# Kernel tuning notes

Hardware: AMD Instinct MI355X
Metric: run time of the kernel (lower is better)

## Reference

```python
import jax, jax.numpy as jnp
import numpy as np

B, D, H, E = 8192, 1024, 4096, 4
LN_EPS = 1e-5


def setup_inputs() -> dict:
    key = jax.random.key(0)
    ks = jax.random.split(key, 10)
    s_gate = 1.0 / np.sqrt(D)
    s1 = 1.0 / np.sqrt(D)
    s2 = 1.0 / np.sqrt(H)
    return {
        "x": jax.random.normal(ks[0], (B, D), dtype=jnp.float32),
        "gate_w": jax.random.uniform(ks[1], (E, D), jnp.float32, -s_gate, s_gate),
        "gate_b": jax.random.uniform(ks[2], (E,), jnp.float32, -s_gate, s_gate),
        "ln_w": jnp.ones((E, D), jnp.float32),
        "ln_b": jnp.zeros((E, D), jnp.float32),
        "w1": jax.random.uniform(ks[3], (E, D, H), jnp.float32, -s1, s1),
        "b1": jax.random.uniform(ks[4], (E, H), jnp.float32, -s1, s1),
        "w2": jax.random.uniform(ks[5], (E, H, D), jnp.float32, -s2, s2),
        "b2": jax.random.uniform(ks[6], (E, D), jnp.float32, -s2, s2),
        "top_k": 2,
    }


def reference(x, gate_w, gate_b, ln_w, ln_b, w1, b1, w2, b2, top_k):
    n_experts = gate_w.shape[0]
    # gating (eval mode: no noise)
    logits = x @ gate_w.T + gate_b            # (B, E)
    probs = jax.nn.softmax(logits, axis=-1)   # (B, E)
    top_w, top_idx = jax.lax.top_k(probs, top_k)  # (B, k)
    top_w = top_w / (jnp.sum(top_w, axis=-1, keepdims=True) + 1e-9)

    # per-expert LayerNorm: shared normalization, per-expert affine
    mu = jnp.mean(x, axis=-1, keepdims=True)
    var = jnp.var(x, axis=-1, keepdims=True)
    xn = (x - mu) * jax.lax.rsqrt(var + LN_EPS)          # (B, D)
    xe = xn[:, None, :] * ln_w[None] + ln_b[None]        # (B, E, D)

    # dense expert MLPs (GELU exact, matching torch nn.GELU default)
    h = jnp.einsum('bed,edh->beh', xe, w1) + b1[None]    # (B, E, H)
    h = jax.nn.gelu(h, approximate=False)
    stacked = jnp.einsum('beh,ehd->bed', h, w2) + b2[None]  # (B, E, D)

    # gather top-k experts and combine
    gathered = jnp.take_along_axis(stacked, top_idx[:, :, None], axis=1)  # (B, k, D)
    y = jnp.sum(gathered * top_w[:, :, None], axis=1)   # (B, D)

    # Switch load-balancing aux loss
    one_hot = jax.nn.one_hot(top_idx, n_experts, dtype=jnp.float32)  # (B, k, E)
    dispatch_frac = jnp.sum(one_hot, axis=(0, 1)) / (x.shape[0] * top_k)
    mean_prob = jnp.mean(probs, axis=0)
    aux = n_experts * jnp.sum(dispatch_frac * mean_prob)

    return y, probs, top_idx, top_w, aux
```

## Files before the change

kernel.cpp:

```cpp
#include <hip/hip_runtime.h>
#include <hip/hip_bf16.h>
#include <math.h>

#define BB 8192
#define DD 1024
#define HH 4096
#define EE 4
#define NT 132
#define CAP (NT * 128)

typedef __attribute__((ext_vector_type(8))) __bf16 bf16x8;
typedef __attribute__((ext_vector_type(4))) float f32x4;

__device__ __forceinline__ unsigned short f2bf(float f) {
    union { float f; unsigned u; } c; c.f = f;
    unsigned u = c.u;
    unsigned r = (u + 0x7FFFu + ((u >> 16) & 1u)) >> 16;
    return (unsigned short)r;
}

__device__ __forceinline__ void load_lds16(const void* g, void* l) {
    __builtin_amdgcn_global_load_lds(
        (const __attribute__((address_space(1))) void*)g,
        (__attribute__((address_space(3))) void*)l, 16, 0, 0);
}

template <int R, int C>
__global__ void k_prep(const float* __restrict__ src, unsigned short* __restrict__ dst) {
    __shared__ unsigned short tileT[64 * 72];
    const int e = blockIdx.z;
    const int r0 = blockIdx.y * 64, c0 = blockIdx.x * 64;
    const float* s = src + (size_t)e * R * C;
    unsigned short* d = dst + (size_t)e * R * C;
    const int tid = threadIdx.x;
    const int cc = (tid & 15) * 4;
#pragma unroll
    for (int it = 0; it < 4; ++it) {
        int rr = (tid >> 4) + it * 16;
        float4 v = *(const float4*)(s + (size_t)(r0 + rr) * C + c0 + cc);
        tileT[(cc + 0) * 72 + rr] = f2bf(v.x);
        tileT[(cc + 1) * 72 + rr] = f2bf(v.y);
        tileT[(cc + 2) * 72 + rr] = f2bf(v.z);
        tileT[(cc + 3) * 72 + rr] = f2bf(v.w);
    }
    __syncthreads();
#pragma unroll
    for (int it = 0; it < 2; ++it) {
        int chunk = tid + it * 256;
        int cl = chunk >> 3, rl = (chunk & 7) * 8;
        uint4 vv = *(const uint4*)&tileT[cl * 72 + rl];
        *(uint4*)(d + (size_t)(c0 + cl) * R + r0 + rl) = vv;
    }
}

__global__ __launch_bounds__(256) void k_gate(
        const float* __restrict__ x, const float* __restrict__ gw,
        const float* __restrict__ gb,
        float* __restrict__ mu, float* __restrict__ rstd,
        int* __restrict__ cnt, int* __restrict__ rows_tmp,
        float* __restrict__ wts_tmp,
        float* __restrict__ probs_out, float* __restrict__ idx_out,
        float* __restrict__ w_out) {
    const int tid = threadIdx.x;
    const int lane = tid & 63, wv = tid >> 6;
    __shared__ int   s_e[64];
    __shared__ float s_w[64];
    __shared__ int   s_pos[64];
    __shared__ int   s_base[4];

    for (int i = 0; i < 8; ++i) {
        const int rloc = wv * 8 + i;
        const int r = blockIdx.x * 32 + rloc;
        float l0 = 0, l1 = 0, l2 = 0, l3 = 0, s = 0, ss = 0;
#pragma unroll
        for (int k = 0; k < 4; ++k) {
            const int off = k * 256 + lane * 4;
            float4 xv = *(const float4*)(x + (size_t)r * DD + off);
            s  += xv.x + xv.y + xv.z + xv.w;
            ss += xv.x * xv.x + xv.y * xv.y + xv.z * xv.z + xv.w * xv.w;
            float4 g0 = *(const float4*)(gw + 0 * DD + off);
            float4 g1 = *(const float4*)(gw + 1 * DD + off);
            float4 g2 = *(const float4*)(gw + 2 * DD + off);
            float4 g3 = *(const float4*)(gw + 3 * DD + off);
            l0 += xv.x * g0.x + xv.y * g0.y + xv.z * g0.z + xv.w * g0.w;
            l1 += xv.x * g1.x + xv.y * g1.y + xv.z * g1.z + xv.w * g1.w;
            l2 += xv.x * g2.x + xv.y * g2.y + xv.z * g2.z + xv.w * g2.w;
            l3 += xv.x * g3.x + xv.y * g3.y + xv.z * g3.z + xv.w * g3.w;
        }
#pragma unroll
        for (int off = 32; off > 0; off >>= 1) {
            l0 += __shfl_xor(l0, off, 64);
            l1 += __shfl_xor(l1, off, 64);
            l2 += __shfl_xor(l2, off, 64);
            l3 += __shfl_xor(l3, off, 64);
            s  += __shfl_xor(s,  off, 64);
            ss += __shfl_xor(ss, off, 64);
        }
        if (lane == 0) {
            float m = s * (1.0f / DD);
            float var = ss * (1.0f / DD) - m * m;
            mu[r] = m;
            rstd[r] = rsqrtf(var + 1e-5f);
            float lg[4] = { l0 + gb[0], l1 + gb[1], l2 + gb[2], l3 + gb[3] };
            float mx = fmaxf(fmaxf(lg[0], lg[1]), fmaxf(lg[2], lg[3]));
            float p[4], tot = 0.f;
#pragma unroll
            for (int e = 0; e < 4; ++e) { p[e] = __expf(lg[e] - mx); tot += p[e]; }
            float inv = 1.0f / tot;
#pragma unroll
            for (int e = 0; e < 4; ++e) { p[e] *= inv; probs_out[(size_t)r * 4 + e] = p[e]; }
            int e0 = 0; float p0 = p[0];
#pragma unroll
            for (int e = 1; e < 4; ++e) if (p[e] > p0) { p0 = p[e]; e0 = e; }
            int e1 = -1; float p1 = -1.f;
#pragma unroll
            for (int e = 0; e < 4; ++e) if (e != e0 && p[e] > p1) { p1 = p[e]; e1 = e; }
            float s2 = 1.0f / (p0 + p1 + 1e-9f);
            float w0 = p0 * s2, w1v = p1 * s2;
            idx_out[r * 2 + 0] = (float)e0;
            idx_out[r * 2 + 1] = (float)e1;
            w_out[r * 2 + 0] = w0;
            w_out[r * 2 + 1] = w1v;
            s_e[rloc * 2 + 0] = e0; s_w[rloc * 2 + 0] = w0;
            s_e[rloc * 2 + 1] = e1; s_w[rloc * 2 + 1] = w1v;
        }
    }
    __syncthreads();
    if (tid < 4) {
        int c = 0;
        for (int k = 0; k < 64; ++k)
            if (s_e[k] == tid) s_pos[k] = c++;
        s_base[tid] = atomicAdd(cnt + tid, c);
    }
    __syncthreads();
    if (tid < 64) {
        int e = s_e[tid];
        int p = s_base[e] + s_pos[tid];
        int r = blockIdx.x * 32 + (tid >> 1);
        rows_tmp[e * BB + p] = r;
        wts_tmp[e * BB + p] = s_w[tid];
    }
}

__global__ void k_aux(const float* __restrict__ probs, const int* __restrict__ cnt,
                      int* __restrict__ aoff, int* __restrict__ tile_e,
                      float* __restrict__ aux_out) {
    const int tid = threadIdx.x;
    float s0 = 0, s1 = 0, s2 = 0, s3 = 0;
    for (int r = tid; r < BB; r += 256) {
        float4 p = *(const float4*)(probs + (size_t)r * 4);
        s0 += p.x; s1 += p.y; s2 += p.z; s3 += p.w;
    }
    __shared__ float red[4][256];
    red[0][tid] = s0; red[1][tid] = s1; red[2][tid] = s2; red[3][tid] = s3;
    __syncthreads();
    for (int off = 128; off > 0; off >>= 1) {
        if (tid < off) {
#pragma unroll
            for (int q = 0; q < 4; ++q) red[q][tid] += red[q][tid + off];
        }
        __syncthreads();
    }
    if (tid == 0) {
        float aux = 0.f;
        for (int e = 0; e < 4; ++e) {
            float mean_p = red[e][0] * (1.0f / BB);
            float frac = (float)cnt[e] * (1.0f / (BB * 2));
            aux += frac * mean_p;
        }
        aux_out[0] = 4.0f * aux;
        int a = 0; aoff[0] = 0;
        for (int e = 0; e < 4; ++e) { a += ((cnt[e] + 127) >> 7) << 7; aoff[e + 1] = a; }
        for (int t = 0; t < NT; ++t) {
            int ee = 0;
            for (int e = 0; e < 4; ++e)
                if (t * 128 >= aoff[e] && t * 128 < aoff[e + 1]) ee = e;
            tile_e[t] = ee;
        }
    }
}

__global__ void k_pack(const float* __restrict__ x, const float* __restrict__ lnw,
                       const float* __restrict__ lnb,
                       const float* __restrict__ mu, const float* __restrict__ rstd,
                       const int* __restrict__ cnt, const int* __restrict__ aoff,
                       const int* __restrict__ tile_e,
                       const int* __restrict__ rows_tmp, const float* __restrict__ wts_tmp,
                       int* __restrict__ row_pk, float* __restrict__ wt_pk,
                       unsigned short* __restrict__ Apk) {
    const int i = blockIdx.x;
    if (i >= aoff[4]) return;
    const int e = tile_e[i >> 7];
    const int j = i - aoff[e];
    const int tid = threadIdx.x;
    unsigned short* dst = Apk + (size_t)i * DD + tid * 4;
    if (j < cnt[e]) {
        int b = rows_tmp[e * BB + j];
        if (tid == 0) { row_pk[i] = b; wt_pk[i] = wts_tmp[e * BB + j]; }
        float m = mu[b], rs = rstd[b];
        float4 xv = *(const float4*)(x + (size_t)b * DD + tid * 4);
        float4 wv = *(const float4*)(lnw + (size_t)e * DD + tid * 4);
        float4 bv = *(const float4*)(lnb + (size_t)e * DD + tid * 4);
        ushort4 o;
        o.x = f2bf((xv.x - m) * rs * wv.x + bv.x);
        o.y = f2bf((xv.y - m) * rs * wv.y + bv.y);
        o.z = f2bf((xv.z - m) * rs * wv.z + bv.z);
        o.w = f2bf((xv.w - m) * rs * wv.w + bv.w);
        *(ushort4*)dst = o;
    } else {
        if (tid == 0) { row_pk[i] = -1; wt_pk[i] = 0.f; }
        ushort4 z; z.x = z.y = z.z = z.w = 0;
        *(ushort4*)dst = z;
    }
}

template <int K, int N, int MODE>
__global__ void moe_gemm(const __bf16* __restrict__ A, const __bf16* __restrict__ W,
                         const float* __restrict__ bias,
                         const int* __restrict__ aoff, const int* __restrict__ tile_e,
                         const int* __restrict__ row_pk, const float* __restrict__ wt_pk,
                         unsigned short* __restrict__ Hout, float* __restrict__ Y) {
    __shared__ __align__(16) __bf16 As[128 * 64];
    __shared__ __align__(16) __bf16 Bs[128 * 64];

    constexpr int NBHALF = N / 128 / 2;
    constexpr int NBGRP  = (NBHALF >= 8) ? 8 : NBHALF;
    const int id = blockIdx.x;
    const int xcd = id & 7, slot = id >> 3;
    const int nbg  = slot / (33 * NBGRP);
    const int rem  = slot - nbg * (33 * NBGRP);
    const int tloc = rem / NBGRP;
    const int nbi  = rem - tloc * NBGRP;
    const int t  = (xcd >> 1) * 33 + tloc;
    const int nb = (xcd & 1) * NBHALF + nbg * NBGRP + nbi;

    if (t * 128 >= aoff[4]) return;
    const int e = tile_e[t];
    const int tid = threadIdx.x;
    const int lane = tid & 63;
    const int wave = tid >> 6;
    const int wm = wave & 1, wn = wave >> 1;
    const int lm = lane & 15, q = lane >> 4;

    const int srow = tid >> 3;
    const int schunk = ((tid & 7) ^ (srow & 7)) * 8;
    const __bf16* Ag = A + (size_t)(t * 128 + srow) * K + schunk;
    const __bf16* Bg = W + (size_t)e * N * K + (size_t)(nb * 128 + srow) * K + schunk;
    __bf16* Al = As + tid * 8;
    __bf16* Bl = Bs + tid * 8;

    f32x4 acc[4][4] = {};
    int arow[4], brow[4];
#pragma unroll
    for (int i = 0; i < 4; ++i) {
        arow[i] = wm * 64 + i * 16 + lm;
        brow[i] = wn * 64 + i * 16 + lm;
    }

    for (int kt = 0; kt < K / 64; ++kt) {
#pragma unroll
        for (int i = 0; i < 4; ++i) load_lds16(Ag + (size_t)i * 32 * K + kt * 64, Al + i * 2048);
#pragma unroll
        for (int i = 0; i < 4; ++i) load_lds16(Bg + (size_t)i * 32 * K + kt * 64, Bl + i * 2048);
        __syncthreads();
#pragma unroll
        for (int kk = 0; kk < 2; ++kk) {
            bf16x8 af[4], bfr[4];
#pragma unroll
            for (int i = 0; i < 4; ++i)
                af[i] = *(const bf16x8*)(As + arow[i] * 64 + (((kk * 4 + q) ^ (arow[i] & 7)) * 8));
#pragma unroll
            for (int j = 0; j < 4; ++j)
                bfr[j] = *(const bf16x8*)(Bs + brow[j] * 64 + (((kk * 4 + q) ^ (brow[j] & 7)) * 8));
#pragma unroll
            for (int i = 0; i < 4; ++i)
#pragma unroll
                for (int j = 0; j < 4; ++j)
                    acc[i][j] = __builtin_amdgcn_mfma_f32_16x16x32_bf16(af[i], bfr[j], acc[i][j], 0, 0, 0);
        }
        __syncthreads();
    }

    if (MODE == 1) {
#pragma unroll
        for (int j = 0; j < 4; ++j) {
            int col = nb * 128 + wn * 64 + j * 16 + lm;
            float bv = bias[e * N + col];
#pragma unroll
            for (int i = 0; i < 4; ++i) {
                int rl = wm * 64 + i * 16 + q * 4;
                size_t base = (size_t)(t * 128 + rl) * N + col;
#pragma unroll
                for (int r = 0; r < 4; ++r) {
                    float v = acc[i][j][r] + bv;
                    float u2 = 2.0f * v * (0.7978845608f + 0.0356774081f * v * v);
                    float g = v / (1.0f + __expf(-u2));
                    Hout[base + (size_t)r * N] = f2bf(g);
                }
            }
        }
    } else {
        float bv[4];
#pragma unroll
        for (int j = 0; j < 4; ++j) bv[j] = bias[e * N + nb * 128 + wn * 64 + j * 16 + lm];
#pragma unroll
        for (int i = 0; i < 4; ++i) {
#pragma unroll
            for (int r = 0; r < 4; ++r) {
                int ig = t * 128 + wm * 64 + i * 16 + q * 4 + r;
                int brw = row_pk[ig];
                if (brw >= 0) {
                    float wgt = wt_pk[ig];
#pragma unroll
                    for (int j = 0; j < 4; ++j) {
                        int col = nb * 128 + wn * 64 + j * 16 + lm;
                        atomicAdd(Y + (size_t)brw * DD + col, (acc[i][j][r] + bv[j]) * wgt);
                    }
                }
            }
        }
    }
}

extern "C" void kernel_launch(void* const* d_in, const int* in_sizes, int n_in,
                              void* d_out, int out_size, void* d_ws, size_t ws_size,
                              hipStream_t stream) {
    const float* x   = (const float*)d_in[0];
    const float* gw  = (const float*)d_in[1];
    const float* gb  = (const float*)d_in[2];
    const float* lnw = (const float*)d_in[3];
    const float* lnb = (const float*)d_in[4];
    const float* w1  = (const float*)d_in[5];
    const float* b1  = (const float*)d_in[6];
    const float* w2  = (const float*)d_in[7];
    const float* b2  = (const float*)d_in[8];
    float* out = (float*)d_out;

    char* ws = (char*)d_ws;
    size_t o = 0;
    auto alloc = [&](size_t bytes) { size_t r = o; o += (bytes + 255) & ~(size_t)255; return r; };
    float* mu       = (float*)(ws + alloc((size_t)BB * 4));
    float* rstd     = (float*)(ws + alloc((size_t)BB * 4));
    int*   cnt      = (int*)(ws + alloc(16));
    int*   aoff     = (int*)(ws + alloc(5 * 4));
    int*   te       = (int*)(ws + alloc(NT * 4));
    int*   rows_tmp = (int*)(ws + alloc((size_t)EE * BB * 4));
    float* wts_tmp  = (float*)(ws + alloc((size_t)EE * BB * 4));
    int*   row_pk   = (int*)(ws + alloc((size_t)CAP * 4));
    float* wt_pk    = (float*)(ws + alloc((size_t)CAP * 4));
    unsigned short* w1t = (unsigned short*)(ws + alloc((size_t)EE * DD * HH * 2));
    unsigned short* w2t = (unsigned short*)(ws + alloc((size_t)EE * DD * HH * 2));
    unsigned short* Apk = (unsigned short*)(ws + alloc((size_t)CAP * DD * 2));
    unsigned short* Hpk = (unsigned short*)(ws + alloc((size_t)CAP * HH * 2));
    if (o > ws_size) return;

    float* y_out     = out;
    float* probs_out = out + (size_t)BB * DD;
    float* idx_out   = probs_out + (size_t)BB * EE;
    float* w_out     = idx_out + (size_t)BB * 2;
    float* aux_out   = w_out + (size_t)BB * 2;

    hipMemsetAsync(y_out, 0, (size_t)BB * DD * 4, stream);
    hipMemsetAsync(cnt, 0, 16, stream);

    k_prep<DD, HH><<<dim3(HH / 64, DD / 64, EE), 256, 0, stream>>>(w1, w1t);
    k_prep<HH, DD><<<dim3(DD / 64, HH / 64, EE), 256, 0, stream>>>(w2, w2t);
    k_gate<<<BB / 32, 256, 0, stream>>>(x, gw, gb, mu, rstd, cnt, rows_tmp, wts_tmp,
                                        probs_out, idx_out, w_out);
    k_aux<<<1, 256, 0, stream>>>(probs_out, cnt, aoff, te, aux_out);
    k_pack<<<CAP, 256, 0, stream>>>(x, lnw, lnb, mu, rstd, cnt, aoff, te,
                                    rows_tmp, wts_tmp, row_pk, wt_pk, Apk);
    moe_gemm<DD, HH, 1><<<8 * 33 * (HH / 256), 256, 0, stream>>>(
        (const __bf16*)Apk, (const __bf16*)w1t, b1, aoff, te, nullptr, nullptr, Hpk, nullptr);
    moe_gemm<HH, DD, 2><<<8 * 33 * (DD / 256), 256, 0, stream>>>(
        (const __bf16*)Hpk, (const __bf16*)w2t, b2, aoff, te, row_pk, wt_pk, nullptr, y_out);
}
```

Measured before the change: 625.3 us.

## Rewrite MoE GEMM as 256x256 double-buffered tiles with split-K for down projection

The grouped expert GEMM now uses 512-thread blocks computing 256x256 tiles, with LDS double buffering. The next K-slice is prefetched in four staged chunks interleaved with MFMA phases, and s_setprio raises wave priority around the math. Expert segments are padded to 256 rows (NT raised to 136). The second GEMM splits K in two and accumulates the halves through the existing atomics. This aims to raise data reuse and overlap global loads with compute, at the cost of more LDS and registers, extra padding work, and twice the atomic traffic in the second GEMM.

Result: slower. 760.8 us (+21.7%).

```diff
diff --git a/kernel.cpp b/kernel.cpp
--- a/kernel.cpp
+++ b/kernel.cpp
@@ -6,7 +6,7 @@
 #define DD 1024
 #define HH 4096
 #define EE 4
-#define NT 132
+#define NT 136
 #define CAP (NT * 128)
 
 typedef __attribute__((ext_vector_type(8))) __bf16 bf16x8;
@@ -23,6 +23,12 @@
     __builtin_amdgcn_global_load_lds(
         (const __attribute__((address_space(1))) void*)g,
         (__attribute__((address_space(3))) void*)l, 16, 0, 0);
+}
+
+__device__ __forceinline__ void tile_sync() {
+    asm volatile("s_waitcnt vmcnt(0)" ::: "memory");
+    __builtin_amdgcn_s_barrier();
+    asm volatile("" ::: "memory");
 }
 
 template <int R, int C>
@@ -170,7 +176,7 @@
         }
         aux_out[0] = 4.0f * aux;
         int a = 0; aoff[0] = 0;
-        for (int e = 0; e < 4; ++e) { a += ((cnt[e] + 127) >> 7) << 7; aoff[e + 1] = a; }
+        for (int e = 0; e < 4; ++e) { a += ((cnt[e] + 255) >> 8) << 8; aoff[e + 1] = a; }
         for (int t = 0; t < NT; ++t) {
             int ee = 0;
             for (int e = 0; e < 4; ++e)
@@ -214,82 +220,163 @@
     }
 }
 
-template <int K, int N, int MODE>
-__global__ void moe_gemm(const __bf16* __restrict__ A, const __bf16* __restrict__ W,
-                         const float* __restrict__ bias,
-                         const int* __restrict__ aoff, const int* __restrict__ tile_e,
-                         const int* __restrict__ row_pk, const float* __restrict__ wt_pk,
-                         unsigned short* __restrict__ Hout, float* __restrict__ Y) {
-    __shared__ __align__(16) __bf16 As[128 * 64];
-    __shared__ __align__(16) __bf16 Bs[128 * 64];
-
-    constexpr int NBHALF = N / 128 / 2;
-    constexpr int NBGRP  = (NBHALF >= 8) ? 8 : NBHALF;
+template <int K, int N, int MODE, int KSPLIT>
+__global__ __launch_bounds__(512, 2) void moe_gemm(
+        const __bf16* __restrict__ A, const __bf16* __restrict__ W,
+        const float* __restrict__ bias,
+        const int* __restrict__ aoff, const int* __restrict__ tile_e,
+        const int* __restrict__ row_pk, const float* __restrict__ wt_pk,
+        unsigned short* __restrict__ Hout, float* __restrict__ Y) {
+    __shared__ __align__(16) __bf16 As[2][256 * 64];
+    __shared__ __align__(16) __bf16 Bs[2][256 * 64];
+
+    constexpr int NBT  = N / 256;
+    constexpr int NBX  = (KSPLIT == 1) ? NBT / 2 : NBT;
+    constexpr int KSEG = K / KSPLIT;
+    constexpr int NKT  = KSEG / 64;
+
     const int id = blockIdx.x;
     const int xcd = id & 7, slot = id >> 3;
-    const int nbg  = slot / (33 * NBGRP);
-    const int rem  = slot - nbg * (33 * NBGRP);
-    const int tloc = rem / NBGRP;
-    const int nbi  = rem - tloc * NBGRP;
-    const int t  = (xcd >> 1) * 33 + tloc;
-    const int nb = (xcd & 1) * NBHALF + nbg * NBGRP + nbi;
-
-    if (t * 128 >= aoff[4]) return;
-    const int e = tile_e[t];
+    const int tloc = slot / NBX, nbi = slot % NBX;
+    const int t  = (xcd >> 1) * 17 + tloc;
+    const int nb = (KSPLIT == 1) ? (xcd & 1) * NBX + nbi : nbi;
+    const int ks = (KSPLIT == 1) ? 0 : (xcd & 1);
+
+    if (t * 256 >= aoff[4]) return;
+    const int e = tile_e[t * 2];
     const int tid = threadIdx.x;
     const int lane = tid & 63;
     const int wave = tid >> 6;
-    const int wm = wave & 1, wn = wave >> 1;
+    const int wm = wave >> 2, wn = wave & 3;
     const int lm = lane & 15, q = lane >> 4;
 
     const int srow = tid >> 3;
     const int schunk = ((tid & 7) ^ (srow & 7)) * 8;
-    const __bf16* Ag = A + (size_t)(t * 128 + srow) * K + schunk;
-    const __bf16* Bg = W + (size_t)e * N * K + (size_t)(nb * 128 + srow) * K + schunk;
-    __bf16* Al = As + tid * 8;
-    __bf16* Bl = Bs + tid * 8;
-
-    f32x4 acc[4][4] = {};
-    int arow[4], brow[4];
-#pragma unroll
-    for (int i = 0; i < 4; ++i) {
-        arow[i] = wm * 64 + i * 16 + lm;
-        brow[i] = wn * 64 + i * 16 + lm;
-    }
-
-    for (int kt = 0; kt < K / 64; ++kt) {
-#pragma unroll
-        for (int i = 0; i < 4; ++i) load_lds16(Ag + (size_t)i * 32 * K + kt * 64, Al + i * 2048);
-#pragma unroll
-        for (int i = 0; i < 4; ++i) load_lds16(Bg + (size_t)i * 32 * K + kt * 64, Bl + i * 2048);
-        __syncthreads();
-#pragma unroll
-        for (int kk = 0; kk < 2; ++kk) {
-            bf16x8 af[4], bfr[4];
+    const __bf16* Ag = A + (size_t)(t * 256 + srow) * K + ks * KSEG + schunk;
+    const __bf16* Bg = W + (size_t)e * N * K + (size_t)(nb * 256 + srow) * K + ks * KSEG + schunk;
+
+    auto stage = [&](int kt1, int bufi, int m) {
+        const int rb = (m & 1) * 128;
+        if (m < 2) {
+            load_lds16(Ag + (size_t)rb * K + kt1 * 64,        &As[bufi][rb * 64] + tid * 8);
+            load_lds16(Ag + (size_t)(rb + 64) * K + kt1 * 64, &As[bufi][(rb + 64) * 64] + tid * 8);
+        } else {
+            load_lds16(Bg + (size_t)rb * K + kt1 * 64,        &Bs[bufi][rb * 64] + tid * 8);
+            load_lds16(Bg + (size_t)(rb + 64) * K + kt1 * 64, &Bs[bufi][(rb + 64) * 64] + tid * 8);
+        }
+    };
+
+    f32x4 acc[8][4] = {};
+
+#pragma unroll
+    for (int m = 0; m < 4; ++m) stage(0, 0, m);
+    tile_sync();
+
+    for (int kt = 0; kt < NKT; ++kt) {
+        const int cur = kt & 1, nxt = cur ^ 1;
+        const __bf16* Ab = &As[cur][0];
+        const __bf16* Bb = &Bs[cur][0];
+        const bool pf = (kt + 1 < NKT);
+
+        bf16x8 a0[4][2], b0[2][2];
+
+#pragma unroll
+        for (int i = 0; i < 4; ++i) {
+            const int r = wm * 128 + i * 16 + lm;
+#pragma unroll
+            for (int kk = 0; kk < 2; ++kk)
+                a0[i][kk] = *(const bf16x8*)(Ab + r * 64 + (((kk * 4 + q) ^ (r & 7)) * 8));
+        }
+#pragma unroll
+        for (int j = 0; j < 2; ++j) {
+            const int r = wn * 64 + j * 16 + lm;
+#pragma unroll
+            for (int kk = 0; kk < 2; ++kk)
+                b0[j][kk] = *(const bf16x8*)(Bb + r * 64 + (((kk * 4 + q) ^ (r & 7)) * 8));
+        }
+        if (pf) stage(kt + 1, nxt, 0);
+        __builtin_amdgcn_s_barrier();
+        __builtin_amdgcn_s_setprio(1);
+#pragma unroll
+        for (int kk = 0; kk < 2; ++kk)
 #pragma unroll
             for (int i = 0; i < 4; ++i)
-                af[i] = *(const bf16x8*)(As + arow[i] * 64 + (((kk * 4 + q) ^ (arow[i] & 7)) * 8));
-#pragma unroll
-            for (int j = 0; j < 4; ++j)
-                bfr[j] = *(const bf16x8*)(Bs + brow[j] * 64 + (((kk * 4 + q) ^ (brow[j] & 7)) * 8));
+#pragma unroll
+                for (int j = 0; j < 2; ++j)
+                    acc[i][j] = __builtin_amdgcn_mfma_f32_16x16x32_bf16(a0[i][kk], b0[j][kk], acc[i][j], 0, 0, 0);
+        __builtin_amdgcn_s_setprio(0);
+        __builtin_amdgcn_s_barrier();
+
+#pragma unroll
+        for (int j = 0; j < 2; ++j) {
+            const int r = wn * 64 + (j + 2) * 16 + lm;
+#pragma unroll
+            for (int kk = 0; kk < 2; ++kk)
+                b0[j][kk] = *(const bf16x8*)(Bb + r * 64 + (((kk * 4 + q) ^ (r & 7)) * 8));
+        }
+        if (pf) stage(kt + 1, nxt, 1);
+        __builtin_amdgcn_s_barrier();
+        __builtin_amdgcn_s_setprio(1);
+#pragma unroll
+        for (int kk = 0; kk < 2; ++kk)
 #pragma unroll
             for (int i = 0; i < 4; ++i)
 #pragma unroll
-                for (int j = 0; j < 4; ++j)
-                    acc[i][j] = __builtin_amdgcn_mfma_f32_16x16x32_bf16(af[i], bfr[j], acc[i][j], 0, 0, 0);
-        }
-        __syncthreads();
+                for (int j = 0; j < 2; ++j)
+                    acc[i][j + 2] = __builtin_amdgcn_mfma_f32_16x16x32_bf16(a0[i][kk], b0[j][kk], acc[i][j + 2], 0, 0, 0);
+        __builtin_amdgcn_s_setprio(0);
+        __builtin_amdgcn_s_barrier();
+
+#pragma unroll
+        for (int i = 0; i < 4; ++i) {
+            const int r = wm * 128 + (i + 4) * 16 + lm;
+#pragma unroll
+            for (int kk = 0; kk < 2; ++kk)
+                a0[i][kk] = *(const bf16x8*)(Ab + r * 64 + (((kk * 4 + q) ^ (r & 7)) * 8));
+        }
+        if (pf) stage(kt + 1, nxt, 2);
+        __builtin_amdgcn_s_barrier();
+        __builtin_amdgcn_s_setprio(1);
+#pragma unroll
+        for (int kk = 0; kk < 2; ++kk)
+#pragma unroll
+            for (int i = 0; i < 4; ++i)
+#pragma unroll
+                for (int j = 0; j < 2; ++j)
+                    acc[i + 4][j + 2] = __builtin_amdgcn_mfma_f32_16x16x32_bf16(a0[i][kk], b0[j][kk], acc[i + 4][j + 2], 0, 0, 0);
+        __builtin_amdgcn_s_setprio(0);
+        __builtin_amdgcn_s_barrier();
+
+#pragma unroll
+        for (int j = 0; j < 2; ++j) {
+            const int r = wn * 64 + j * 16 + lm;
+#pragma unroll
+            for (int kk = 0; kk < 2; ++kk)
+                b0[j][kk] = *(const bf16x8*)(Bb + r * 64 + (((kk * 4 + q) ^ (r & 7)) * 8));
+        }
+        if (pf) stage(kt + 1, nxt, 3);
+        __builtin_amdgcn_s_barrier();
+        __builtin_amdgcn_s_setprio(1);
+#pragma unroll
+        for (int kk = 0; kk < 2; ++kk)
+#pragma unroll
+            for (int i = 0; i < 4; ++i)
+#pragma unroll
+                for (int j = 0; j < 2; ++j)
+                    acc[i + 4][j] = __builtin_amdgcn_mfma_f32_16x16x32_bf16(a0[i][kk], b0[j][kk], acc[i + 4][j], 0, 0, 0);
+        __builtin_amdgcn_s_setprio(0);
+        tile_sync();
     }
 
     if (MODE == 1) {
 #pragma unroll
         for (int j = 0; j < 4; ++j) {
-            int col = nb * 128 + wn * 64 + j * 16 + lm;
-            float bv = bias[e * N + col];
-#pragma unroll
-            for (int i = 0; i < 4; ++i) {
-                int rl = wm * 64 + i * 16 + q * 4;
-                size_t base = (size_t)(t * 128 + rl) * N + col;
+            const int col = nb * 256 + wn * 64 + j * 16 + lm;
+            const float bv = bias[e * N + col];
+#pragma unroll
+            for (int i = 0; i < 8; ++i) {
+                const int rl = wm * 128 + i * 16 + q * 4;
+                const size_t base = (size_t)(t * 256 + rl) * N + col;
 #pragma unroll
                 for (int r = 0; r < 4; ++r) {
                     float v = acc[i][j][r] + bv;
@@ -302,18 +389,19 @@
     } else {
         float bv[4];
 #pragma unroll
-        for (int j = 0; j < 4; ++j) bv[j] = bias[e * N + nb * 128 + wn * 64 + j * 16 + lm];
-#pragma unroll
-        for (int i = 0; i < 4; ++i) {
+        for (int j = 0; j < 4; ++j)
+            bv[j] = (ks == 0) ? bias[e * N + nb * 256 + wn * 64 + j * 16 + lm] : 0.f;
+#pragma unroll
+        for (int i = 0; i < 8; ++i) {
 #pragma unroll
             for (int r = 0; r < 4; ++r) {
-                int ig = t * 128 + wm * 64 + i * 16 + q * 4 + r;
-                int brw = row_pk[ig];
+                const int ig = t * 256 + wm * 128 + i * 16 + q * 4 + r;
+                const int brw = row_pk[ig];
                 if (brw >= 0) {
-                    float wgt = wt_pk[ig];
+                    const float wgt = wt_pk[ig];
 #pragma unroll
                     for (int j = 0; j < 4; ++j) {
-                        int col = nb * 128 + wn * 64 + j * 16 + lm;
+                        const int col = nb * 256 + wn * 64 + j * 16 + lm;
                         atomicAdd(Y + (size_t)brw * DD + col, (acc[i][j][r] + bv[j]) * wgt);
                     }
                 }
@@ -370,8 +458,8 @@
     k_aux<<<1, 256, 0, stream>>>(probs_out, cnt, aoff, te, aux_out);
     k_pack<<<CAP, 256, 0, stream>>>(x, lnw, lnb, mu, rstd, cnt, aoff, te,
                                     rows_tmp, wts_tmp, row_pk, wt_pk, Apk);
-    moe_gemm<DD, HH, 1><<<8 * 33 * (HH / 256), 256, 0, stream>>>(
+    moe_gemm<DD, HH, 1, 1><<<8 * 17 * (HH / 256 / 2), 512, 0, stream>>>(
         (const __bf16*)Apk, (const __bf16*)w1t, b1, aoff, te, nullptr, nullptr, Hpk, nullptr);
-    moe_gemm<HH, DD, 2><<<8 * 33 * (DD / 256), 256, 0, stream>>>(
+    moe_gemm<HH, DD, 2, 2><<<8 * 17 * (DD / 256), 512, 0, stream>>>(
         (const __bf16*)Hpk, (const __bf16*)w2t, b2, aoff, te, row_pk, wt_pk, nullptr, y_out);
 }
```

## Use 256x256 tiles with 4-stage async LDS pipeline and split-K for down-projection

Applied to the files above, without the earlier changes.

Rewrites the expert GEMM to 256x256 output tiles computed by 512 threads, with a 4-deep ring of LDS buffers loaded via global_load_lds and explicit vmcnt waits so loads overlap MFMA work. Expert padding becomes 256-row aligned and the tile count is raised accordingly. The second GEMM splits K across two blocks that both atomically accumulate into the output, with bias added only by the first. The aim is more data reuse per tile and latency hiding; in exchange it uses more padding rows, more registers, doubles the atomic traffic on the second GEMM, and shares LDS/occupancy across larger blocks.

New measurement: 753.9 us. 1.21x slower.

```diff
diff --git a/kernel.cpp b/kernel.cpp
--- a/kernel.cpp
+++ b/kernel.cpp
@@ -6,7 +6,7 @@
 #define DD 1024
 #define HH 4096
 #define EE 4
-#define NT 132
+#define NT 136
 #define CAP (NT * 128)
 
 typedef __attribute__((ext_vector_type(8))) __bf16 bf16x8;
@@ -170,7 +170,7 @@
         }
         aux_out[0] = 4.0f * aux;
         int a = 0; aoff[0] = 0;
-        for (int e = 0; e < 4; ++e) { a += ((cnt[e] + 127) >> 7) << 7; aoff[e + 1] = a; }
+        for (int e = 0; e < 4; ++e) { a += ((cnt[e] + 255) >> 8) << 8; aoff[e + 1] = a; }
         for (int t = 0; t < NT; ++t) {
             int ee = 0;
             for (int e = 0; e < 4; ++e)
@@ -214,82 +214,95 @@
     }
 }
 
-template <int K, int N, int MODE>
-__global__ void moe_gemm(const __bf16* __restrict__ A, const __bf16* __restrict__ W,
-                         const float* __restrict__ bias,
-                         const int* __restrict__ aoff, const int* __restrict__ tile_e,
-                         const int* __restrict__ row_pk, const float* __restrict__ wt_pk,
-                         unsigned short* __restrict__ Hout, float* __restrict__ Y) {
-    __shared__ __align__(16) __bf16 As[128 * 64];
-    __shared__ __align__(16) __bf16 Bs[128 * 64];
-
-    constexpr int NBHALF = N / 128 / 2;
-    constexpr int NBGRP  = (NBHALF >= 8) ? 8 : NBHALF;
+template <int K, int N, int MODE, int KSPLIT>
+__global__ __launch_bounds__(512, 2) void moe_gemm(
+        const __bf16* __restrict__ A, const __bf16* __restrict__ W,
+        const float* __restrict__ bias,
+        const int* __restrict__ aoff, const int* __restrict__ tile_e,
+        const int* __restrict__ row_pk, const float* __restrict__ wt_pk,
+        unsigned short* __restrict__ Hout, float* __restrict__ Y) {
+    __shared__ __align__(16) __bf16 As[4][256 * 32];
+    __shared__ __align__(16) __bf16 Bs[4][256 * 32];
+
+    constexpr int NBT  = N / 256;
+    constexpr int NBX  = (KSPLIT == 1) ? NBT / 2 : NBT;
+    constexpr int KSEG = K / KSPLIT;
+    constexpr int NKT  = KSEG / 32;
+
     const int id = blockIdx.x;
     const int xcd = id & 7, slot = id >> 3;
-    const int nbg  = slot / (33 * NBGRP);
-    const int rem  = slot - nbg * (33 * NBGRP);
-    const int tloc = rem / NBGRP;
-    const int nbi  = rem - tloc * NBGRP;
-    const int t  = (xcd >> 1) * 33 + tloc;
-    const int nb = (xcd & 1) * NBHALF + nbg * NBGRP + nbi;
-
-    if (t * 128 >= aoff[4]) return;
-    const int e = tile_e[t];
+    const int tloc = slot / NBX, nbi = slot % NBX;
+    const int t  = (xcd >> 1) * 17 + tloc;
+    const int nb = (KSPLIT == 1) ? (xcd & 1) * NBX + nbi : nbi;
+    const int ks = (KSPLIT == 1) ? 0 : (xcd & 1);
+
+    if (t * 256 >= aoff[4]) return;
+    const int e = tile_e[t * 2];
     const int tid = threadIdx.x;
     const int lane = tid & 63;
     const int wave = tid >> 6;
-    const int wm = wave & 1, wn = wave >> 1;
+    const int wm = wave >> 2, wn = wave & 3;
     const int lm = lane & 15, q = lane >> 4;
 
-    const int srow = tid >> 3;
-    const int schunk = ((tid & 7) ^ (srow & 7)) * 8;
-    const __bf16* Ag = A + (size_t)(t * 128 + srow) * K + schunk;
-    const __bf16* Bg = W + (size_t)e * N * K + (size_t)(nb * 128 + srow) * K + schunk;
-    __bf16* Al = As + tid * 8;
-    __bf16* Bl = Bs + tid * 8;
-
-    f32x4 acc[4][4] = {};
-    int arow[4], brow[4];
-#pragma unroll
-    for (int i = 0; i < 4; ++i) {
-        arow[i] = wm * 64 + i * 16 + lm;
-        brow[i] = wn * 64 + i * 16 + lm;
-    }
-
-    for (int kt = 0; kt < K / 64; ++kt) {
-#pragma unroll
-        for (int i = 0; i < 4; ++i) load_lds16(Ag + (size_t)i * 32 * K + kt * 64, Al + i * 2048);
-#pragma unroll
-        for (int i = 0; i < 4; ++i) load_lds16(Bg + (size_t)i * 32 * K + kt * 64, Bl + i * 2048);
-        __syncthreads();
-#pragma unroll
-        for (int kk = 0; kk < 2; ++kk) {
-            bf16x8 af[4], bfr[4];
-#pragma unroll
-            for (int i = 0; i < 4; ++i)
-                af[i] = *(const bf16x8*)(As + arow[i] * 64 + (((kk * 4 + q) ^ (arow[i] & 7)) * 8));
+    const int srow = tid >> 2;
+    const int schunk = ((tid & 3) ^ (srow & 3)) * 8;
+    const __bf16* Ag = A + (size_t)(t * 256 + srow) * K + ks * KSEG + schunk;
+    const __bf16* Bg = W + (size_t)e * N * K + (size_t)(nb * 256 + srow) * K + ks * KSEG + schunk;
+
+    f32x4 acc[8][4] = {};
+
+#define STAGE(kt1) do { \
+        const int _b = (kt1) & 3; \
+        load_lds16(Ag + (size_t)(kt1) * 32,           &As[_b][0]    + tid * 8); \
+        load_lds16(Ag + 128 * (size_t)K + (kt1) * 32, &As[_b][4096] + tid * 8); \
+        load_lds16(Bg + (size_t)(kt1) * 32,           &Bs[_b][0]    + tid * 8); \
+        load_lds16(Bg + 128 * (size_t)K + (kt1) * 32, &Bs[_b][4096] + tid * 8); \
+    } while (0)
+
+    STAGE(0); STAGE(1); STAGE(2);
+
+#pragma unroll 1
+    for (int kt = 0; kt < NKT; ++kt) {
+        const int rem = NKT - 1 - kt;
+        if (rem >= 2)      asm volatile("s_waitcnt vmcnt(8)" ::: "memory");
+        else if (rem == 1) asm volatile("s_waitcnt vmcnt(4)" ::: "memory");
+        else               asm volatile("s_waitcnt vmcnt(0)" ::: "memory");
+        __builtin_amdgcn_s_barrier();
+        asm volatile("" ::: "memory");
+
+        const __bf16* Ab = &As[kt & 3][0];
+        const __bf16* Bb = &Bs[kt & 3][0];
+        bf16x8 af[8], bfr[4];
+#pragma unroll
+        for (int i = 0; i < 8; ++i) {
+            const int r = wm * 128 + i * 16 + lm;
+            af[i] = *(const bf16x8*)(Ab + r * 32 + ((q ^ (r & 3)) * 8));
+        }
+#pragma unroll
+        for (int j = 0; j < 4; ++j) {
+            const int r = wn * 64 + j * 16 + lm;
+            bfr[j] = *(const bf16x8*)(Bb + r * 32 + ((q ^ (r & 3)) * 8));
+        }
+        if (kt + 3 < NKT) STAGE(kt + 3);
+        __builtin_amdgcn_s_setprio(1);
+#pragma unroll
+        for (int i = 0; i < 8; ++i)
 #pragma unroll
             for (int j = 0; j < 4; ++j)
-                bfr[j] = *(const bf16x8*)(Bs + brow[j] * 64 + (((kk * 4 + q) ^ (brow[j] & 7)) * 8));
-#pragma unroll
-            for (int i = 0; i < 4; ++i)
-#pragma unroll
-                for (int j = 0; j < 4; ++j)
-                    acc[i][j] = __builtin_amdgcn_mfma_f32_16x16x32_bf16(af[i], bfr[j], acc[i][j], 0, 0, 0);
-        }
-        __syncthreads();
-    }
+                acc[i][j] = __builtin_amdgcn_mfma_f32_16x16x32_bf16(af[i], bfr[j], acc[i][j], 0, 0, 0);
+        __builtin_amdgcn_s_setprio(0);
+    }
+#undef STAGE
 
     if (MODE == 1) {
 #pragma unroll
         for (int j = 0; j < 4; ++j) {
-            int col = nb * 128 + wn * 64 + j * 16 + lm;
-            float bv = bias[e * N + col];
-#pragma unroll
-            for (int i = 0; i < 4; ++i) {
-                int rl = wm * 64 + i * 16 + q * 4;
-                size_t base = (size_t)(t * 128 + rl) * N + col;
+            const int col = nb * 256 + wn * 64 + j * 16 + lm;
+            const float bv = bias[e * N + col];
+#pragma unroll
+            for (int i = 0; i < 8; ++i) {
+                const int rl = wm * 128 + i * 16 + q * 4;
+                const size_t base = (size_t)(t * 256 + rl) * N + col;
 #pragma unroll
                 for (int r = 0; r < 4; ++r) {
                     float v = acc[i][j][r] + bv;
@@ -302,18 +315,19 @@
     } else {
         float bv[4];
 #pragma unroll
-        for (int j = 0; j < 4; ++j) bv[j] = bias[e * N + nb * 128 + wn * 64 + j * 16 + lm];
-#pragma unroll
-        for (int i = 0; i < 4; ++i) {
+        for (int j = 0; j < 4; ++j)
+            bv[j] = (ks == 0) ? bias[e * N + nb * 256 + wn * 64 + j * 16 + lm] : 0.f;
+#pragma unroll
+        for (int i = 0; i < 8; ++i) {
 #pragma unroll
             for (int r = 0; r < 4; ++r) {
-                int ig = t * 128 + wm * 64 + i * 16 + q * 4 + r;
-                int brw = row_pk[ig];
+                const int ig = t * 256 + wm * 128 + i * 16 + q * 4 + r;
+                const int brw = row_pk[ig];
                 if (brw >= 0) {
-                    float wgt = wt_pk[ig];
+                    const float wgt = wt_pk[ig];
 #pragma unroll
                     for (int j = 0; j < 4; ++j) {
-                        int col = nb * 128 + wn * 64 + j * 16 + lm;
+                        const int col = nb * 256 + wn * 64 + j * 16 + lm;
                         atomicAdd(Y + (size_t)brw * DD + col, (acc[i][j][r] + bv[j]) * wgt);
                     }
                 }
@@ -370,8 +384,8 @@
     k_aux<<<1, 256, 0, stream>>>(probs_out, cnt, aoff, te, aux_out);
     k_pack<<<CAP, 256, 0, stream>>>(x, lnw, lnb, mu, rstd, cnt, aoff, te,
                                     rows_tmp, wts_tmp, row_pk, wt_pk, Apk);
-    moe_gemm<DD, HH, 1><<<8 * 33 * (HH / 256), 256, 0, stream>>>(
+    moe_gemm<DD, HH, 1, 1><<<8 * 17 * (HH / 256 / 2), 512, 0, stream>>>(
         (const __bf16*)Apk, (const __bf16*)w1t, b1, aoff, te, nullptr, nullptr, Hpk, nullptr);
-    moe_gemm<HH, DD, 2><<<8 * 33 * (DD / 256), 256, 0, stream>>>(
+    moe_gemm<HH, DD, 2, 2><<<8 * 17 * (DD / 256), 512, 0, stream>>>(
         (const __bf16*)Hpk, (const __bf16*)w2t, b2, aoff, te, row_pk, wt_pk, nullptr, y_out);
 }
```

## Fuse setup kernels: merge weight preps, fold aux into gate, zero y in pack

Applied to the files above, without the earlier changes.

The two weight-transpose kernels are merged into one launch, which also zeroes the counters. The aux-loss and tile-offset computation moves into the gate kernel: each block atomically accumulates its probability sums and the last block to finish computes the offsets. The y memset is folded into the pack kernel, which now handles four rows per block with one wavefront per row. The aim is fewer launches and memsets and less per-launch overhead, at the cost of extra atomics and a last-block-done pattern that relies on threadfence ordering.

New measurement: 650.3 us. 1.04x slower.

```diff
diff --git a/kernel.cpp b/kernel.cpp
--- a/kernel.cpp
+++ b/kernel.cpp
@@ -25,14 +25,32 @@
         (__attribute__((address_space(3))) void*)l, 16, 0, 0);
 }
 
-template <int R, int C>
-__global__ void k_prep(const float* __restrict__ src, unsigned short* __restrict__ dst) {
+__global__ void k_prep(const float* __restrict__ w1, const float* __restrict__ w2,
+                       unsigned short* __restrict__ w1t, unsigned short* __restrict__ w2t,
+                       int* __restrict__ cnt, float* __restrict__ psum,
+                       int* __restrict__ done) {
     __shared__ unsigned short tileT[64 * 72];
-    const int e = blockIdx.z;
-    const int r0 = blockIdx.y * 64, c0 = blockIdx.x * 64;
-    const float* s = src + (size_t)e * R * C;
-    unsigned short* d = dst + (size_t)e * R * C;
     const int tid = threadIdx.x;
+    if (blockIdx.x == 0 && blockIdx.y == 0 && blockIdx.z == 0) {
+        if (tid < 4) cnt[tid] = 0;
+        else if (tid < 8) psum[tid - 4] = 0.f;
+        else if (tid == 8) done[0] = 0;
+    }
+    const int z = blockIdx.z;
+    const float* s;
+    unsigned short* d;
+    int R, C, r0, c0;
+    if (z < 4) {
+        s = w1 + (size_t)z * DD * HH;  d = w1t + (size_t)z * DD * HH;
+        R = DD; C = HH;
+        r0 = blockIdx.y * 64; c0 = blockIdx.x * 64;
+    } else {
+        const int e = z - 4;
+        s = w2 + (size_t)e * DD * HH;  d = w2t + (size_t)e * DD * HH;
+        R = HH; C = DD;
+        const int idx = blockIdx.y * 64 + blockIdx.x;
+        c0 = (idx & 15) * 64; r0 = (idx >> 4) * 64;
+    }
     const int cc = (tid & 15) * 4;
 #pragma unroll
     for (int it = 0; it < 4; ++it) {
@@ -57,16 +75,22 @@
         const float* __restrict__ x, const float* __restrict__ gw,
         const float* __restrict__ gb,
         float* __restrict__ mu, float* __restrict__ rstd,
-        int* __restrict__ cnt, int* __restrict__ rows_tmp,
-        float* __restrict__ wts_tmp,
+        int* __restrict__ cnt, float* __restrict__ psum, int* __restrict__ done,
+        int* __restrict__ rows_tmp, float* __restrict__ wts_tmp,
         float* __restrict__ probs_out, float* __restrict__ idx_out,
-        float* __restrict__ w_out) {
+        float* __restrict__ w_out,
+        int* __restrict__ aoff, int* __restrict__ tile_e,
+        float* __restrict__ aux_out) {
     const int tid = threadIdx.x;
     const int lane = tid & 63, wv = tid >> 6;
     __shared__ int   s_e[64];
     __shared__ float s_w[64];
     __shared__ int   s_pos[64];
     __shared__ int   s_base[4];
+    __shared__ float s_ps[4][4];
+    __shared__ int   s_last;
+
+    float lp0 = 0.f, lp1 = 0.f, lp2 = 0.f, lp3 = 0.f;
 
     for (int i = 0; i < 8; ++i) {
         const int rloc = wv * 8 + i;
@@ -109,6 +133,7 @@
             float inv = 1.0f / tot;
 #pragma unroll
             for (int e = 0; e < 4; ++e) { p[e] *= inv; probs_out[(size_t)r * 4 + e] = p[e]; }
+            lp0 += p[0]; lp1 += p[1]; lp2 += p[2]; lp3 += p[3];
             int e0 = 0; float p0 = p[0];
 #pragma unroll
             for (int e = 1; e < 4; ++e) if (p[e] > p0) { p0 = p[e]; e0 = e; }
@@ -125,12 +150,16 @@
             s_e[rloc * 2 + 1] = e1; s_w[rloc * 2 + 1] = w1v;
         }
     }
+    if (lane == 0) {
+        s_ps[wv][0] = lp0; s_ps[wv][1] = lp1; s_ps[wv][2] = lp2; s_ps[wv][3] = lp3;
+    }
     __syncthreads();
     if (tid < 4) {
         int c = 0;
         for (int k = 0; k < 64; ++k)
             if (s_e[k] == tid) s_pos[k] = c++;
         s_base[tid] = atomicAdd(cnt + tid, c);
+        atomicAdd(psum + tid, s_ps[0][tid] + s_ps[1][tid] + s_ps[2][tid] + s_ps[3][tid]);
     }
     __syncthreads();
     if (tid < 64) {
@@ -140,37 +169,21 @@
         rows_tmp[e * BB + p] = r;
         wts_tmp[e * BB + p] = s_w[tid];
     }
-}
-
-__global__ void k_aux(const float* __restrict__ probs, const int* __restrict__ cnt,
-                      int* __restrict__ aoff, int* __restrict__ tile_e,
-                      float* __restrict__ aux_out) {
-    const int tid = threadIdx.x;
-    float s0 = 0, s1 = 0, s2 = 0, s3 = 0;
-    for (int r = tid; r < BB; r += 256) {
-        float4 p = *(const float4*)(probs + (size_t)r * 4);
-        s0 += p.x; s1 += p.y; s2 += p.z; s3 += p.w;
-    }
-    __shared__ float red[4][256];
-    red[0][tid] = s0; red[1][tid] = s1; red[2][tid] = s2; red[3][tid] = s3;
+    __threadfence();
     __syncthreads();
-    for (int off = 128; off > 0; off >>= 1) {
-        if (tid < off) {
-#pragma unroll
-            for (int q = 0; q < 4; ++q) red[q][tid] += red[q][tid + off];
-        }
-        __syncthreads();
-    }
-    if (tid == 0) {
+    if (tid == 0) s_last = atomicAdd(done, 1);
+    __syncthreads();
+    if (s_last == (int)gridDim.x - 1 && tid == 0) {
+        int c[4];
+        for (int e = 0; e < 4; ++e) c[e] = atomicAdd(cnt + e, 0);
         float aux = 0.f;
+        int a = 0; aoff[0] = 0;
         for (int e = 0; e < 4; ++e) {
-            float mean_p = red[e][0] * (1.0f / BB);
-            float frac = (float)cnt[e] * (1.0f / (BB * 2));
-            aux += frac * mean_p;
+            float mean_p = atomicAdd(psum + e, 0.f) * (1.0f / BB);
+            aux += ((float)c[e] * (1.0f / (BB * 2))) * mean_p;
+            a += ((c[e] + 127) >> 7) << 7; aoff[e + 1] = a;
         }
         aux_out[0] = 4.0f * aux;
-        int a = 0; aoff[0] = 0;
-        for (int e = 0; e < 4; ++e) { a += ((cnt[e] + 127) >> 7) << 7; aoff[e + 1] = a; }
         for (int t = 0; t < NT; ++t) {
             int ee = 0;
             for (int e = 0; e < 4; ++e)
@@ -180,37 +193,50 @@
     }
 }
 
-__global__ void k_pack(const float* __restrict__ x, const float* __restrict__ lnw,
-                       const float* __restrict__ lnb,
-                       const float* __restrict__ mu, const float* __restrict__ rstd,
-                       const int* __restrict__ cnt, const int* __restrict__ aoff,
-                       const int* __restrict__ tile_e,
-                       const int* __restrict__ rows_tmp, const float* __restrict__ wts_tmp,
-                       int* __restrict__ row_pk, float* __restrict__ wt_pk,
-                       unsigned short* __restrict__ Apk) {
-    const int i = blockIdx.x;
+__global__ __launch_bounds__(256) void k_pack(
+        const float* __restrict__ x, const float* __restrict__ lnw,
+        const float* __restrict__ lnb,
+        const float* __restrict__ mu, const float* __restrict__ rstd,
+        const int* __restrict__ cnt, const int* __restrict__ aoff,
+        const int* __restrict__ tile_e,
+        const int* __restrict__ rows_tmp, const float* __restrict__ wts_tmp,
+        int* __restrict__ row_pk, float* __restrict__ wt_pk,
+        unsigned short* __restrict__ Apk, float* __restrict__ y) {
+    const int blk = blockIdx.x, tid = threadIdx.x;
+    const int wv = tid >> 6, lane = tid & 63;
+    if (blk < BB / 4) {
+        float4 z4; z4.x = z4.y = z4.z = z4.w = 0.f;
+        float* yr = y + (size_t)(blk * 4 + wv) * DD + lane * 4;
+#pragma unroll
+        for (int k = 0; k < 4; ++k) *(float4*)(yr + k * 256) = z4;
+    }
+    const int i = blk * 4 + wv;
     if (i >= aoff[4]) return;
     const int e = tile_e[i >> 7];
     const int j = i - aoff[e];
-    const int tid = threadIdx.x;
-    unsigned short* dst = Apk + (size_t)i * DD + tid * 4;
+    unsigned short* dst = Apk + (size_t)i * DD;
     if (j < cnt[e]) {
         int b = rows_tmp[e * BB + j];
-        if (tid == 0) { row_pk[i] = b; wt_pk[i] = wts_tmp[e * BB + j]; }
+        if (lane == 0) { row_pk[i] = b; wt_pk[i] = wts_tmp[e * BB + j]; }
         float m = mu[b], rs = rstd[b];
-        float4 xv = *(const float4*)(x + (size_t)b * DD + tid * 4);
-        float4 wv = *(const float4*)(lnw + (size_t)e * DD + tid * 4);
-        float4 bv = *(const float4*)(lnb + (size_t)e * DD + tid * 4);
-        ushort4 o;
-        o.x = f2bf((xv.x - m) * rs * wv.x + bv.x);
-        o.y = f2bf((xv.y - m) * rs * wv.y + bv.y);
-        o.z = f2bf((xv.z - m) * rs * wv.z + bv.z);
-        o.w = f2bf((xv.w - m) * rs * wv.w + bv.w);
-        *(ushort4*)dst = o;
+#pragma unroll
+        for (int k = 0; k < 4; ++k) {
+            const int off = k * 256 + lane * 4;
+            float4 xv = *(const float4*)(x + (size_t)b * DD + off);
+            float4 wv4 = *(const float4*)(lnw + (size_t)e * DD + off);
+            float4 bv4 = *(const float4*)(lnb + (size_t)e * DD + off);
+            ushort4 o;
+            o.x = f2bf((xv.x - m) * rs * wv4.x + bv4.x);
+            o.y = f2bf((xv.y - m) * rs * wv4.y + bv4.y);
+            o.z = f2bf((xv.z - m) * rs * wv4.z + bv4.z);
+            o.w = f2bf((xv.w - m) * rs * wv4.w + bv4.w);
+            *(ushort4*)(dst + off) = o;
+        }
     } else {
-        if (tid == 0) { row_pk[i] = -1; wt_pk[i] = 0.f; }
+        if (lane == 0) { row_pk[i] = -1; wt_pk[i] = 0.f; }
         ushort4 z; z.x = z.y = z.z = z.w = 0;
-        *(ushort4*)dst = z;
+#pragma unroll
+        for (int k = 0; k < 4; ++k) *(ushort4*)(dst + k * 256 + lane * 4) = z;
     }
 }
 
@@ -342,6 +368,8 @@
     float* mu       = (float*)(ws + alloc((size_t)BB * 4));
     float* rstd     = (float*)(ws + alloc((size_t)BB * 4));
     int*   cnt      = (int*)(ws + alloc(16));
+    float* psum     = (float*)(ws + alloc(16));
+    int*   done     = (int*)(ws + alloc(16));
     int*   aoff     = (int*)(ws + alloc(5 * 4));
     int*   te       = (int*)(ws + alloc(NT * 4));
     int*   rows_tmp = (int*)(ws + alloc((size_t)EE * BB * 4));
@@ -360,16 +388,12 @@
     float* w_out     = idx_out + (size_t)BB * 2;
     float* aux_out   = w_out + (size_t)BB * 2;
 
-    hipMemsetAsync(y_out, 0, (size_t)BB * DD * 4, stream);
-    hipMemsetAsync(cnt, 0, 16, stream);
-
-    k_prep<DD, HH><<<dim3(HH / 64, DD / 64, EE), 256, 0, stream>>>(w1, w1t);
-    k_prep<HH, DD><<<dim3(DD / 64, HH / 64, EE), 256, 0, stream>>>(w2, w2t);
-    k_gate<<<BB / 32, 256, 0, stream>>>(x, gw, gb, mu, rstd, cnt, rows_tmp, wts_tmp,
-                                        probs_out, idx_out, w_out);
-    k_aux<<<1, 256, 0, stream>>>(probs_out, cnt, aoff, te, aux_out);
-    k_pack<<<CAP, 256, 0, stream>>>(x, lnw, lnb, mu, rstd, cnt, aoff, te,
-                                    rows_tmp, wts_tmp, row_pk, wt_pk, Apk);
+    k_prep<<<dim3(64, 16, 8), 256, 0, stream>>>(w1, w2, w1t, w2t, cnt, psum, done);
+    k_gate<<<BB / 32, 256, 0, stream>>>(x, gw, gb, mu, rstd, cnt, psum, done,
+                                        rows_tmp, wts_tmp, probs_out, idx_out, w_out,
+                                        aoff, te, aux_out);
+    k_pack<<<CAP / 4, 256, 0, stream>>>(x, lnw, lnb, mu, rstd, cnt, aoff, te,
+                                        rows_tmp, wts_tmp, row_pk, wt_pk, Apk, y_out);
     moe_gemm<DD, HH, 1><<<8 * 33 * (HH / 256), 256, 0, stream>>>(
         (const __bf16*)Apk, (const __bf16*)w1t, b1, aoff, te, nullptr, nullptr, Hpk, nullptr);
     moe_gemm<HH, DD, 2><<<8 * 33 * (DD / 256), 256, 0, stream>>>(
```
